# Kernel tuning notes

Hardware: AMD Instinct MI355X
Metric: run time of the kernel (lower is better)

Reference implementation:

```python
import jax, jax.numpy as jnp
import numpy as np

D_MODEL = 256
NUM_ITERS = 5
REG = 0.1
EPS = 1e-12  # torch F.normalize eps


def setup_inputs() -> dict:
    key = jax.random.key(0)
    k1, k2, k3, k4, k5, k6 = jax.random.split(key, 6)
    B, Nd, Ns, D = 16, 1024, 1024, D_MODEL
    bound = 1.0 / np.sqrt(D)
    return {
        "drone_tokens": jax.random.normal(k1, (B, Nd, D), dtype=jnp.float32),
        "sat_tokens": jax.random.normal(k2, (B, Ns, D), dtype=jnp.float32),
        "Wq": jax.random.uniform(k3, (D, D), jnp.float32, -bound, bound),
        "bq": jax.random.uniform(k4, (D,), jnp.float32, -bound, bound),
        "Wk": jax.random.uniform(k5, (D, D), jnp.float32, -bound, bound),
        "bk": jax.random.uniform(k6, (D,), jnp.float32, -bound, bound),
    }


def _l2_normalize(x):
    # matches torch F.normalize(dim=-1): x / max(||x||, eps)
    n = jnp.linalg.norm(x, axis=-1, keepdims=True)
    return x / jnp.maximum(n, EPS)


def reference(drone_tokens, sat_tokens, Wq, bq, Wk, bk):
    # nn.Linear: x @ W^T + b
    q = _l2_normalize(drone_tokens @ Wq.T + bq)   # [B, Nd, D]
    k = _l2_normalize(sat_tokens @ Wk.T + bk)     # [B, Ns, D]
    cost = 1.0 - jnp.einsum("bnd,bmd->bnm", q, k)  # [B, Nd, Ns]
    M = -cost / REG
    for _ in range(NUM_ITERS):
        M = M - jax.scipy.special.logsumexp(M, axis=2, keepdims=True)
        M = M - jax.scipy.special.logsumexp(M, axis=1, keepdims=True)
    transport_plan = jnp.exp(M)
    ot_cost = jnp.mean(jnp.sum(transport_plan * cost, axis=(1, 2)))
    return transport_plan, ot_cost
```

## Files before the change

### kernel.cpp

```cpp
#include <hip/hip_runtime.h>
#include <hip/hip_bf16.h>

#define BATCH 16
#define NQ    1024
#define DM    256
#define NROWS (BATCH * NQ)
#define RINV  10.0f

typedef float  f32x4 __attribute__((ext_vector_type(4)));
typedef short  s16x8 __attribute__((ext_vector_type(8)));

static __device__ __forceinline__ ushort f2bf(float f) {
    unsigned u = __builtin_bit_cast(unsigned, f);
    u += 0x7fffu + ((u >> 16) & 1u);
    return (ushort)(u >> 16);
}
static __device__ __forceinline__ float bf2f(ushort h) {
    return __builtin_bit_cast(float, ((unsigned)h) << 16);
}


__global__ void __launch_bounds__(256) k_prep(const float* __restrict__ Wq,
                                              const float* __restrict__ Wk,
                                              ushort* __restrict__ wp0,
                                              ushort* __restrict__ wp1) {
    int gid = blockIdx.x * 256 + threadIdx.x;
    const float* Wsrc = (gid < 8192) ? Wq : Wk;
    ushort* dst = (gid < 8192) ? wp0 : wp1;
    int gx = gid & 8191;
    int gcol = gx >> 9, kk = (gx >> 6) & 7, ln = gx & 63;
    const float* srow = Wsrc + (size_t)(gcol * 16 + (ln & 15)) * DM
                             + kk * 32 + (ln >> 4) * 8;
    ushort* d = dst + (size_t)gx * 8;
#pragma unroll
    for (int e = 0; e < 8; e++) d[e] = f2bf(srow[e]);
}

__global__ void __launch_bounds__(256) k_proj(
        const float* __restrict__ drone, const float* __restrict__ sat,
        const ushort* __restrict__ wp0, const ushort* __restrict__ wp1,
        const float* __restrict__ bq, const float* __restrict__ bk,
        ushort* __restrict__ qkp) {
    __shared__ union {
        float  As[16][260];
        ushort S[16][280];
    } AB;
    __shared__ float red[4][16];

    int t = threadIdx.x;
    int lane = t & 63, w = t >> 6, l16 = lane & 15, lh = lane >> 4;
    int g = blockIdx.x;
    int row0 = g * 16;
    const float* x; const ushort* Wp; const float* bias; int rsrc;
    if (row0 < NROWS) { x = drone; Wp = wp0; bias = bq; rsrc = row0; }
    else              { x = sat;   Wp = wp1; bias = bk; rsrc = row0 - NROWS; }

    {
        int r = t >> 4, c0 = (t & 15) * 4;
        const float* gp = x + (size_t)(rsrc + r) * DM;
#pragma unroll
        for (int j = 0; j < 4; j++)
            *(f32x4*)&AB.As[r][c0 + j * 64] = *(const f32x4*)(gp + c0 + j * 64);
    }
    __syncthreads();

    f32x4 acc[4];
#pragma unroll
    for (int ni = 0; ni < 4; ni++) acc[ni] = f32x4{0.f, 0.f, 0.f, 0.f};
#pragma unroll
    for (int kk = 0; kk < 8; kk++) {
        int k0 = kk * 32 + lh * 8;
        f32x4 a0 = *(const f32x4*)&AB.As[l16][k0];
        f32x4 a1 = *(const f32x4*)&AB.As[l16][k0 + 4];
        s16x8 av;
#pragma unroll
        for (int j = 0; j < 4; j++) {
            av[j]     = (short)f2bf(a0[j]);
            av[j + 4] = (short)f2bf(a1[j]);
        }
#pragma unroll
        for (int ni = 0; ni < 4; ni++) {
            s16x8 bv = *(const s16x8*)(Wp + ((size_t)((w * 4 + ni) * 8 + kk) * 64 + lane) * 8);
            acc[ni] = __builtin_amdgcn_mfma_f32_16x16x32_bf16(av, bv, acc[ni], 0, 0, 0);
        }
    }
    float ssq[4] = {0.f, 0.f, 0.f, 0.f};
#pragma unroll
    for (int ni = 0; ni < 4; ni++) {
        float bcol = bias[w * 64 + ni * 16 + l16];
#pragma unroll
        for (int r = 0; r < 4; r++) {
            acc[ni][r] += bcol;
            ssq[r] += acc[ni][r] * acc[ni][r];
        }
    }
#pragma unroll
    for (int off = 1; off < 16; off <<= 1)
#pragma unroll
        for (int r = 0; r < 4; r++) ssq[r] += __shfl_xor(ssq[r], off);
    if (l16 == 0)
#pragma unroll
        for (int r = 0; r < 4; r++) red[w][lh * 4 + r] = ssq[r];
    __syncthreads();

    float inv[4];
#pragma unroll
    for (int r = 0; r < 4; r++) {
        int row = lh * 4 + r;
        float tot = red[0][row] + red[1][row] + red[2][row] + red[3][row];
        inv[r] = 1.0f / fmaxf(sqrtf(tot), 1e-12f);
    }
#pragma unroll
    for (int ni = 0; ni < 4; ni++)
#pragma unroll
        for (int r = 0; r < 4; r++)
            AB.S[lh * 4 + r][w * 64 + ni * 16 + l16] = f2bf(acc[ni][r] * inv[r]);
    __syncthreads();
#pragma unroll
    for (int h = 0; h < 2; h++) {
        int kk = w + h * 4;
        s16x8 vv = *(const s16x8*)&AB.S[l16][kk * 32 + lh * 8];
        *(s16x8*)(qkp + ((size_t)(g * 8 + kk) * 64 + lane) * 8) = vv;
    }
}

__global__ void __launch_bounds__(256) k_cost(const ushort* __restrict__ qkp,
                                              char* __restrict__ ktc, int kstride) {
    int t = threadIdx.x, lane = t & 63, w = t >> 6;
    int l16 = lane & 15, lh = lane >> 4;
    int tile = blockIdx.x;
    int b = tile >> 6, ty = (tile >> 3) & 7, tx = tile & 7;
    int rg  = b * 64 + ty * 8 + (w >> 1) * 4;
    int cgp = 1024 + b * 64 + tx * 8 + (w & 1) * 4;
    f32x4 acc[4][4];
#pragma unroll
    for (int i = 0; i < 4; i++)
#pragma unroll
        for (int j = 0; j < 4; j++) acc[i][j] = f32x4{0.f, 0.f, 0.f, 0.f};
#pragma unroll
    for (int kk = 0; kk < 8; kk++) {
        s16x8 am[4], bn[4];
#pragma unroll
        for (int mi = 0; mi < 4; mi++)
            am[mi] = *(const s16x8*)(qkp + ((size_t)((rg + mi) * 8 + kk) * 64 + lane) * 8);
#pragma unroll
        for (int ni = 0; ni < 4; ni++)
            bn[ni] = *(const s16x8*)(qkp + ((size_t)((cgp + ni) * 8 + kk) * 64 + lane) * 8);
#pragma unroll
        for (int mi = 0; mi < 4; mi++)
#pragma unroll
            for (int ni = 0; ni < 4; ni++)
                acc[mi][ni] = __builtin_amdgcn_mfma_f32_16x16x32_bf16(
                    am[mi], bn[ni], acc[mi][ni], 0, 0, 0);
    }
    int rl = ty * 128 + (w >> 1) * 64, cl = tx * 128 + (w & 1) * 64;
#pragma unroll
    for (int mi = 0; mi < 4; mi++)
#pragma unroll
        for (int r = 0; r < 4; r++) {
            int row = rl + mi * 16 + lh * 4 + r;
            ushort* orow = (ushort*)(ktc + (size_t)(b * NQ + row) * (size_t)kstride);
#pragma unroll
            for (int ni = 0; ni < 4; ni++)
                orow[cl + ni * 16 + l16] =
                    f2bf(__expf(fmaf(RINV, acc[mi][ni][r], -RINV)));
        }
}

template<int FIRST>
__global__ void __launch_bounds__(512, 4) k_sink(const char* __restrict__ ktc, int kstride,
                                                 const float* __restrict__ partin,
                                                 float* __restrict__ u,
                                                 float* __restrict__ partout) {
    __shared__ float bsh[NQ];
    __shared__ float pcol[8][NQ];
    int bid = blockIdx.x, t = threadIdx.x;
    int lane = t & 63, w = t >> 6;
    int b = bid >> 5, ch = bid & 31;

    if (FIRST) {
        bsh[t * 2] = 1.0f; bsh[t * 2 + 1] = 1.0f;
    } else {
        float2 s = float2{0.f, 0.f};
        const float* pb = partin + (size_t)b * 32 * NQ + t * 2;
#pragma unroll 8
        for (int c = 0; c < 32; c++) {
            float2 v = *(const float2*)(pb + (size_t)c * NQ);
            s.x += v.x; s.y += v.y;
        }
        bsh[t * 2]     = 1.0f / s.x;
        bsh[t * 2 + 1] = 1.0f / s.y;
    }
    __syncthreads();

    float br0[8], br1[8];
#pragma unroll
    for (int j = 0; j < 8; j++) {
        br0[j] = bsh[lane * 8 + j];
        br1[j] = bsh[512 + lane * 8 + j];
    }

    float pa0[8], pa1[8];
#pragma unroll
    for (int j = 0; j < 8; j++) { pa0[j] = 0.f; pa1[j] = 0.f; }

    int rowbase = (b << 10) + ch * 32 + w * 4;
#pragma unroll
    for (int rp = 0; rp < 2; rp++) {
        const ushort* ra = (const ushort*)(ktc + (size_t)(rowbase + rp * 2) * (size_t)kstride);
        const ushort* rb = (const ushort*)(ktc + (size_t)(rowbase + rp * 2 + 1) * (size_t)kstride);
        s16x8 ka0 = *(const s16x8*)(ra + lane * 8);
        s16x8 ka1 = *(const s16x8*)(ra + 512 + lane * 8);
        s16x8 kb0 = *(const s16x8*)(rb + lane * 8);
        s16x8 kb1 = *(const s16x8*)(rb + 512 + lane * 8);
        float sa = 0.f, sb = 0.f;
#pragma unroll
        for (int j = 0; j < 8; j++) {
            sa = fmaf(bf2f((ushort)ka0[j]), br0[j], sa);
            sa = fmaf(bf2f((ushort)ka1[j]), br1[j], sa);
            sb = fmaf(bf2f((ushort)kb0[j]), br0[j], sb);
            sb = fmaf(bf2f((ushort)kb1[j]), br1[j], sb);
        }
#pragma unroll
        for (int o = 32; o; o >>= 1) {
            sa += __shfl_xor(sa, o);
            sb += __shfl_xor(sb, o);
        }
        float aa = 1.0f / sa, ab = 1.0f / sb;
        if (lane == 0) {
            u[rowbase + rp * 2]     = aa;
            u[rowbase + rp * 2 + 1] = ab;
        }
#pragma unroll
        for (int j = 0; j < 8; j++) {
            pa0[j] = fmaf(bf2f((ushort)ka0[j]), aa, pa0[j]);
            pa0[j] = fmaf(bf2f((ushort)kb0[j]), ab, pa0[j]);
            pa1[j] = fmaf(bf2f((ushort)ka1[j]), aa, pa1[j]);
            pa1[j] = fmaf(bf2f((ushort)kb1[j]), ab, pa1[j]);
        }
    }
#pragma unroll
    for (int j = 0; j < 8; j++) {
        pcol[w][lane * 8 + j]       = pa0[j];
        pcol[w][512 + lane * 8 + j] = pa1[j];
    }
    __syncthreads();
    {
        float2 s = float2{0.f, 0.f};
#pragma unroll
        for (int k = 0; k < 8; k++) {
            s.x += pcol[k][t * 2];
            s.y += pcol[k][t * 2 + 1];
        }
        *(float2*)&partout[((size_t)b * 32 + ch) * NQ + t * 2] = s;
    }
}

__global__ void __launch_bounds__(512) k_final(const char* __restrict__ ktc, int kstride,
                                               const float* __restrict__ partin,
                                               const float* __restrict__ u,
                                               float* __restrict__ out,
                                               float* __restrict__ bprt) {
    __shared__ float bsh[NQ];
    __shared__ float red[8];
    int bid = blockIdx.x, t = threadIdx.x;
    int lane = t & 63, w = t >> 6;
    int b = bid >> 5, ch = bid & 31;
    {
        float2 s = float2{0.f, 0.f};
        const float* pb = partin + (size_t)b * 32 * NQ + t * 2;
#pragma unroll 8
        for (int c = 0; c < 32; c++) {
            float2 v = *(const float2*)(pb + (size_t)c * NQ);
            s.x += v.x; s.y += v.y;
        }
        bsh[t * 2]     = 1.0f / s.x;
        bsh[t * 2 + 1] = 1.0f / s.y;
    }
    __syncthreads();

    float br0[8], br1[8];
#pragma unroll
    for (int j = 0; j < 8; j++) {
        br0[j] = bsh[lane * 8 + j];
        br1[j] = bsh[512 + lane * 8 + j];
    }
    float sacc = 0.f;
    int rowbase = (b << 10) + ch * 32 + w * 4;
#pragma unroll
    for (int rr = 0; rr < 4; rr++) {
        int row = rowbase + rr;
        const ushort* kr = (const ushort*)(ktc + (size_t)row * (size_t)kstride);
        s16x8 k0 = *(const s16x8*)(kr + lane * 8);
        s16x8 k1 = *(const s16x8*)(kr + 512 + lane * 8);
        float a = u[row];
        float* orow = out + (size_t)row * NQ;
        float pv0[8], pv1[8];
#pragma unroll
        for (int j = 0; j < 8; j++) {
            float kf0 = bf2f((ushort)k0[j]);
            float kf1 = bf2f((ushort)k1[j]);
            float p0 = a * br0[j] * kf0;
            float p1 = a * br1[j] * kf1;
            sacc = fmaf(p0, -0.1f * __logf(kf0), sacc);
            sacc = fmaf(p1, -0.1f * __logf(kf1), sacc);
            pv0[j] = p0; pv1[j] = p1;
        }
        *(f32x4*)(orow + lane * 8)           = *(f32x4*)&pv0[0];
        *(f32x4*)(orow + lane * 8 + 4)       = *(f32x4*)&pv0[4];
        *(f32x4*)(orow + 512 + lane * 8)     = *(f32x4*)&pv1[0];
        *(f32x4*)(orow + 512 + lane * 8 + 4) = *(f32x4*)&pv1[4];
    }
#pragma unroll
    for (int o = 32; o; o >>= 1) sacc += __shfl_xor(sacc, o);
    if (lane == 0) red[w] = sacc;
    __syncthreads();
    if (t == 0) {
        float s = 0.f;
#pragma unroll
        for (int k = 0; k < 8; k++) s += red[k];
        bprt[bid] = s;
    }
}

__global__ void k_reduce(const float* __restrict__ bprt, float* __restrict__ out) {
    int t = threadIdx.x;
    float s = bprt[t] + bprt[t + 256];
#pragma unroll
    for (int o = 32; o; o >>= 1) s += __shfl_xor(s, o);
    __shared__ float sm[4];
    if ((t & 63) == 0) sm[t >> 6] = s;
    __syncthreads();
    if (t == 0)
        out[(size_t)BATCH * NQ * NQ] =
            (sm[0] + sm[1] + sm[2] + sm[3]) * (1.0f / BATCH);
}

extern "C" void kernel_launch(void* const* d_in, const int* in_sizes, int n_in,
                              void* d_out, int out_size, void* d_ws, size_t ws_size,
                              hipStream_t stream) {
    const float* drone = (const float*)d_in[0];
    const float* sat   = (const float*)d_in[1];
    const float* Wq    = (const float*)d_in[2];
    const float* bq    = (const float*)d_in[3];
    const float* Wk    = (const float*)d_in[4];
    const float* bk    = (const float*)d_in[5];
    float* out = (float*)d_out;

    char* ws = (char*)d_ws;
    ushort* wp0   = (ushort*)ws;
    ushort* wp1   = (ushort*)(ws + 131072);
    ushort* qkp   = (ushort*)(ws + 262144);
    float*  u     = (float*)(ws + 17039360);
    float*  partA = (float*)(ws + 17104896);
    float*  partB = (float*)(ws + 19202048);
    float*  bprt  = (float*)(ws + 21299200);

    char* ktc; int kstride;
    if (ws_size >= (size_t)54000000) { ktc = ws + 21303296; kstride = 2048; }
    else                             { ktc = (char*)d_out;  kstride = 4096; }

    k_prep<<<64, 256, 0, stream>>>(Wq, Wk, wp0, wp1);
    k_proj<<<2048, 256, 0, stream>>>(drone, sat, wp0, wp1, bq, bk, qkp);
    k_cost<<<1024, 256, 0, stream>>>(qkp, ktc, kstride);

    k_sink<1><<<512, 512, 0, stream>>>(ktc, kstride, nullptr, u, partA);
    k_sink<0><<<512, 512, 0, stream>>>(ktc, kstride, partA, u, partB);
    k_sink<0><<<512, 512, 0, stream>>>(ktc, kstride, partB, u, partA);
    k_sink<0><<<512, 512, 0, stream>>>(ktc, kstride, partA, u, partB);
    k_sink<0><<<512, 512, 0, stream>>>(ktc, kstride, partB, u, partA);

    k_final<<<512, 512, 0, stream>>>(ktc, kstride, partA, u, out, bprt);
    k_reduce<<<1, 256, 0, stream>>>(bprt, out);
}
```

Baseline: 126.0 us.

## Use 1024-thread Sinkhorn blocks with 64 rows each and nontemporal output stores

Sinkhorn and final kernels now launch 256 blocks of 1024 threads, each covering 64 rows instead of 32. This halves the number of column partial sums written and re-read between iterations (16 chunks per batch instead of 32). The final kernel writes the transport plan with nontemporal stores to avoid polluting cache. In exchange, there are fewer blocks (256 on a large GPU), larger LDS use (pcol grows to 64KB) and lower occupancy, which may reduce latency hiding.

```diff
diff --git a/kernel.cpp b/kernel.cpp
--- a/kernel.cpp
+++ b/kernel.cpp
@@ -168,28 +168,25 @@
 }
 
 template<int FIRST>
-__global__ void __launch_bounds__(512, 4) k_sink(const char* __restrict__ ktc, int kstride,
-                                                 const float* __restrict__ partin,
-                                                 float* __restrict__ u,
-                                                 float* __restrict__ partout) {
+__global__ void __launch_bounds__(1024) k_sink(const char* __restrict__ ktc, int kstride,
+                                               const float* __restrict__ partin,
+                                               float* __restrict__ u,
+                                               float* __restrict__ partout) {
     __shared__ float bsh[NQ];
-    __shared__ float pcol[8][NQ];
-    int bid = blockIdx.x, t = threadIdx.x;
+    __shared__ float pcol[16][NQ];
+    int t = threadIdx.x;
     int lane = t & 63, w = t >> 6;
-    int b = bid >> 5, ch = bid & 31;
+    int bid = blockIdx.x;
+    int b = bid >> 4, ch = bid & 15;
 
     if (FIRST) {
-        bsh[t * 2] = 1.0f; bsh[t * 2 + 1] = 1.0f;
+        bsh[t] = 1.0f;
     } else {
-        float2 s = float2{0.f, 0.f};
-        const float* pb = partin + (size_t)b * 32 * NQ + t * 2;
-#pragma unroll 8
-        for (int c = 0; c < 32; c++) {
-            float2 v = *(const float2*)(pb + (size_t)c * NQ);
-            s.x += v.x; s.y += v.y;
-        }
-        bsh[t * 2]     = 1.0f / s.x;
-        bsh[t * 2 + 1] = 1.0f / s.y;
+        const float* pb = partin + (size_t)b * 16 * NQ + t;
+        float s = 0.f;
+#pragma unroll
+        for (int c = 0; c < 16; c++) s += pb[(size_t)c * NQ];
+        bsh[t] = 1.0f / s;
     }
     __syncthreads();
 
@@ -204,7 +201,7 @@
 #pragma unroll
     for (int j = 0; j < 8; j++) { pa0[j] = 0.f; pa1[j] = 0.f; }
 
-    int rowbase = (b << 10) + ch * 32 + w * 4;
+    int rowbase = (b << 10) + ch * 64 + w * 4;
 #pragma unroll
     for (int rp = 0; rp < 2; rp++) {
         const ushort* ra = (const ushort*)(ktc + (size_t)(rowbase + rp * 2) * (size_t)kstride);
@@ -246,36 +243,30 @@
     }
     __syncthreads();
     {
-        float2 s = float2{0.f, 0.f};
-#pragma unroll
-        for (int k = 0; k < 8; k++) {
-            s.x += pcol[k][t * 2];
-            s.y += pcol[k][t * 2 + 1];
-        }
-        *(float2*)&partout[((size_t)b * 32 + ch) * NQ + t * 2] = s;
-    }
-}
-
-__global__ void __launch_bounds__(512) k_final(const char* __restrict__ ktc, int kstride,
-                                               const float* __restrict__ partin,
-                                               const float* __restrict__ u,
-                                               float* __restrict__ out,
-                                               float* __restrict__ bprt) {
+        float s = 0.f;
+#pragma unroll
+        for (int k = 0; k < 16; k++) s += pcol[k][t];
+        partout[((size_t)b * 16 + ch) * NQ + t] = s;
+    }
+}
+
+__global__ void __launch_bounds__(1024) k_final(const char* __restrict__ ktc, int kstride,
+                                                const float* __restrict__ partin,
+                                                const float* __restrict__ u,
+                                                float* __restrict__ out,
+                                                float* __restrict__ bprt) {
     __shared__ float bsh[NQ];
-    __shared__ float red[8];
-    int bid = blockIdx.x, t = threadIdx.x;
+    __shared__ float red[16];
+    int t = threadIdx.x;
     int lane = t & 63, w = t >> 6;
-    int b = bid >> 5, ch = bid & 31;
+    int bid = blockIdx.x;
+    int b = bid >> 4, ch = bid & 15;
     {
-        float2 s = float2{0.f, 0.f};
-        const float* pb = partin + (size_t)b * 32 * NQ + t * 2;
-#pragma unroll 8
-        for (int c = 0; c < 32; c++) {
-            float2 v = *(const float2*)(pb + (size_t)c * NQ);
-            s.x += v.x; s.y += v.y;
-        }
-        bsh[t * 2]     = 1.0f / s.x;
-        bsh[t * 2 + 1] = 1.0f / s.y;
+        const float* pb = partin + (size_t)b * 16 * NQ + t;
+        float s = 0.f;
+#pragma unroll
+        for (int c = 0; c < 16; c++) s += pb[(size_t)c * NQ];
+        bsh[t] = 1.0f / s;
     }
     __syncthreads();
 
@@ -286,7 +277,7 @@
         br1[j] = bsh[512 + lane * 8 + j];
     }
     float sacc = 0.f;
-    int rowbase = (b << 10) + ch * 32 + w * 4;
+    int rowbase = (b << 10) + ch * 64 + w * 4;
 #pragma unroll
     for (int rr = 0; rr < 4; rr++) {
         int row = rowbase + rr;
@@ -306,10 +297,10 @@
             sacc = fmaf(p1, -0.1f * __logf(kf1), sacc);
             pv0[j] = p0; pv1[j] = p1;
         }
-        *(f32x4*)(orow + lane * 8)           = *(f32x4*)&pv0[0];
-        *(f32x4*)(orow + lane * 8 + 4)       = *(f32x4*)&pv0[4];
-        *(f32x4*)(orow + 512 + lane * 8)     = *(f32x4*)&pv1[0];
-        *(f32x4*)(orow + 512 + lane * 8 + 4) = *(f32x4*)&pv1[4];
+        __builtin_nontemporal_store(*(f32x4*)&pv0[0], (f32x4*)(orow + lane * 8));
+        __builtin_nontemporal_store(*(f32x4*)&pv0[4], (f32x4*)(orow + lane * 8 + 4));
+        __builtin_nontemporal_store(*(f32x4*)&pv1[0], (f32x4*)(orow + 512 + lane * 8));
+        __builtin_nontemporal_store(*(f32x4*)&pv1[4], (f32x4*)(orow + 512 + lane * 8 + 4));
     }
 #pragma unroll
     for (int o = 32; o; o >>= 1) sacc += __shfl_xor(sacc, o);
@@ -318,14 +309,14 @@
     if (t == 0) {
         float s = 0.f;
 #pragma unroll
-        for (int k = 0; k < 8; k++) s += red[k];
+        for (int k = 0; k < 16; k++) s += red[k];
         bprt[bid] = s;
     }
 }
 
 __global__ void k_reduce(const float* __restrict__ bprt, float* __restrict__ out) {
     int t = threadIdx.x;
-    float s = bprt[t] + bprt[t + 256];
+    float s = bprt[t];
 #pragma unroll
     for (int o = 32; o; o >>= 1) s += __shfl_xor(s, o);
     __shared__ float sm[4];
@@ -364,12 +355,12 @@
     k_proj<<<2048, 256, 0, stream>>>(drone, sat, wp0, wp1, bq, bk, qkp);
     k_cost<<<1024, 256, 0, stream>>>(qkp, ktc, kstride);
 
-    k_sink<1><<<512, 512, 0, stream>>>(ktc, kstride, nullptr, u, partA);
-    k_sink<0><<<512, 512, 0, stream>>>(ktc, kstride, partA, u, partB);
-    k_sink<0><<<512, 512, 0, stream>>>(ktc, kstride, partB, u, partA);
-    k_sink<0><<<512, 512, 0, stream>>>(ktc, kstride, partA, u, partB);
-    k_sink<0><<<512, 512, 0, stream>>>(ktc, kstride, partB, u, partA);
-
-    k_final<<<512, 512, 0, stream>>>(ktc, kstride, partA, u, out, bprt);
+    k_sink<1><<<256, 1024, 0, stream>>>(ktc, kstride, nullptr, u, partA);
+    k_sink<0><<<256, 1024, 0, stream>>>(ktc, kstride, partA, u, partB);
+    k_sink<0><<<256, 1024, 0, stream>>>(ktc, kstride, partB, u, partA);
+    k_sink<0><<<256, 1024, 0, stream>>>(ktc, kstride, partA, u, partB);
+    k_sink<0><<<256, 1024, 0, stream>>>(ktc, kstride, partB, u, partA);
+
+    k_final<<<256, 1024, 0, stream>>>(ktc, kstride, partA, u, out, bprt);
     k_reduce<<<1, 256, 0, stream>>>(bprt, out);
 }
```

Result: slower. 129.0 us (+2.4%).
